# Optimization experiments

Hardware: AMD Instinct MI355X
Metric: run time of the kernel (lower is better)

Reference implementation:

```python
import jax, jax.numpy as jnp
import numpy as np

B, S, I, H = 64, 512, 1024, 1024

def setup_inputs() -> dict:
    key = jax.random.key(0)
    k1, k2, k3 = jax.random.split(key, 3)
    scale = 1.0 / np.sqrt(I + H)
    x = jax.random.normal(k1, (B, S, I), dtype=jnp.float32)
    # Stacked gate weights, order: [cell_candidate, forget, update, output]
    W = jax.random.normal(k2, (4 * H, I + H), dtype=jnp.float32) * scale
    b = jax.random.normal(k3, (4 * H,), dtype=jnp.float32) * scale
    return {"x": x, "W": W, "b": b}

def _lstm(x, W, b):
    Wx = W[:, :I]   # (4H, I)
    Wh = W[:, I:]   # (4H, H)
    # Precompute input contribution for all timesteps in one big GEMM
    xW = jnp.einsum('bsi,gi->bsg', x, Wx) + b  # (B, S, 4H)
    xW_t = jnp.transpose(xW, (1, 0, 2))        # (S, B, 4H)

    def step(carry, xw):
        h, c = carry
        pre = xw + h @ Wh.T                    # (B, 4H)
        cand, f, u, o = jnp.split(pre, 4, axis=-1)
        cand = jnp.tanh(cand)
        f = jax.nn.sigmoid(f)
        u = jax.nn.sigmoid(u)
        o = jax.nn.sigmoid(o)
        c = u * cand + f * c
        h = o * jnp.tanh(c)
        return (h, c), h

    h0 = jnp.zeros((x.shape[0], H), dtype=x.dtype)
    c0 = jnp.zeros((x.shape[0], H), dtype=x.dtype)
    (h_n, c_n), outs = jax.lax.scan(step, (h0, c0), xW_t)
    output_seq = jnp.transpose(outs, (1, 0, 2))  # (B, S, H)
    return output_seq, h_n[None], c_n[None]

def reference(x, W, b):
    return _lstm(x, W, b)
```

## Files before the change

kernel.cpp:

```cpp
#include <hip/hip_runtime.h>
#include <math.h>

typedef unsigned short ushort_t;
typedef unsigned long long u64;
typedef __attribute__((ext_vector_type(4))) float f32x4;
typedef __attribute__((ext_vector_type(8))) short s16x8;

#define XW_OFF   0UL
#define XB_OFF   268435456UL
#define WXP_OFF  335544320UL
#define WHP_OFF  343932928UL
#define BP_OFF   352321536UL
#define HBUF_OFF 352337920UL
#define CNT_OFF  352600064UL

__device__ __forceinline__ ushort_t f2bf(float f) {
  unsigned u = __builtin_bit_cast(unsigned, f);
  unsigned r = u + 0x7FFFu + ((u >> 16) & 1u);
  return (ushort_t)(r >> 16);
}
__device__ __forceinline__ float bf2f(ushort_t h) {
  unsigned u = ((unsigned)h) << 16;
  return __builtin_bit_cast(float, u);
}
__device__ __forceinline__ float sigm(float x) { return 1.f / (1.f + __expf(-x)); }
__device__ __forceinline__ float tanh_f(float x) {
  float t = __expf(-2.f * fabsf(x));
  float r = (1.f - t) / (1.f + t);
  return x >= 0.f ? r : -r;
}
__device__ __forceinline__ void gload_lds16(const void* g, void* l) {
  __builtin_amdgcn_global_load_lds(
      (const __attribute__((address_space(1))) unsigned int*)g,
      (__attribute__((address_space(3))) unsigned int*)l, 16, 0, 0);
}

__global__ __launch_bounds__(256) void convert_x(const float* __restrict__ x,
                                                 ushort_t* __restrict__ xb) {
  long gid = (long)blockIdx.x * 256 + threadIdx.x;
  const float4* x4 = (const float4*)x;
  float4 f0 = x4[gid * 2];
  float4 f1 = x4[gid * 2 + 1];
  s16x8 o;
  o[0] = (short)f2bf(f0.x); o[1] = (short)f2bf(f0.y);
  o[2] = (short)f2bf(f0.z); o[3] = (short)f2bf(f0.w);
  o[4] = (short)f2bf(f1.x); o[5] = (short)f2bf(f1.y);
  o[6] = (short)f2bf(f1.z); o[7] = (short)f2bf(f1.w);
  ((s16x8*)xb)[gid] = o;
}

__global__ __launch_bounds__(256) void prep_pack(const float* __restrict__ W,
                                                 const float* __restrict__ bias,
                                                 ushort_t* __restrict__ wxp,
                                                 ushort_t* __restrict__ whp,
                                                 float* __restrict__ bp,
                                                 ushort_t* __restrict__ hbuf,
                                                 int* __restrict__ cnt) {
  long gid = (long)blockIdx.x * 256 + threadIdx.x;
  if (gid < 524288) {
    int l = gid & 63, kc = (int)((gid >> 6) & 31), w = (int)((gid >> 11) & 3);
    int kb = (int)(gid >> 13);
    int li = l & 15, quad = l >> 4;
    int colb = w * 16 + li;
    int G = (colb & 3) * 1024 + kb * 16 + (colb >> 2);
    int kk = kc * 32 + quad * 8;
    const float* src = W + (long)G * 2048 + 1024 + kk;
    ushort_t* dst = whp + gid * 8;
#pragma unroll
    for (int j = 0; j < 8; ++j) dst[j] = f2bf(src[j]);
  } else if (gid < 1048576) {
    long id = gid - 524288;
    int k8 = (int)(id & 127);
    int R = (int)(id >> 7);
    int c = R & 63, kb = R >> 6;
    int G = (c & 3) * 1024 + kb * 16 + (c >> 2);
    const float* src = W + (long)G * 2048 + k8 * 8;
    ushort_t* dst = wxp + (long)R * 1024 + k8 * 8;
#pragma unroll
    for (int j = 0; j < 8; ++j) dst[j] = f2bf(src[j]);
  } else if (gid < 1048576 + 4096) {
    int R = (int)(gid - 1048576);
    int c = R & 63, kb = R >> 6;
    int G = (c & 3) * 1024 + kb * 16 + (c >> 2);
    bp[R] = bias[G];
  } else if (gid < 1048576 + 4096 + 8192) {
    long id = gid - 1048576 - 4096;
    s16x8 z = {0, 0, 0, 0, 0, 0, 0, 0};
    ((s16x8*)hbuf)[id] = z;
  } else if (gid < 1048576 + 4096 + 8192 + 2048) {
    cnt[gid - 1048576 - 4096 - 8192] = 0;
  }
}

__global__ __launch_bounds__(256) void lstm_phase1(const ushort_t* __restrict__ xb,
                                                   const ushort_t* __restrict__ wxp,
                                                   const float* __restrict__ bp,
                                                   ushort_t* __restrict__ xw) {
  __shared__ ushort_t As[16 * 512];
  __shared__ ushort_t Bs[16 * 512];
  int bid = blockIdx.x;
  int nt = bid & 31, mtb = bid >> 5;
  int n0 = nt * 128;
  int t0 = mtb * 2;
  int tid = threadIdx.x, w = tid >> 6, l = tid & 63;
  int quad = l >> 4, li = l & 15;
  int mh = w & 1, nh = w >> 1;
  f32x4 acc[4][4] = {};

  for (int k0 = 0; k0 < 1024; k0 += 64) {
    __syncthreads();
#pragma unroll
    for (int i = 0; i < 4; ++i) {
      int c = w * 4 + i;
      int mt = c >> 1, kcl = c & 1;
      int r = mt * 16 + li;
      int tt = t0 + (r >> 6), bb = r & 63;
      gload_lds16(xb + (long)(bb * 512 + tt) * 1024 + k0 + kcl * 32 + quad * 8,
                  &As[c * 512]);
      int rn = n0 + mt * 16 + li;
      gload_lds16(wxp + (long)rn * 1024 + k0 + kcl * 32 + quad * 8, &Bs[c * 512]);
    }
    __syncthreads();
#pragma unroll
    for (int kcl = 0; kcl < 2; ++kcl) {
      s16x8 av[4], bv[4];
#pragma unroll
      for (int i = 0; i < 4; ++i)
        av[i] = *(const s16x8*)&As[((mh * 4 + i) * 2 + kcl) * 512 + l * 8];
#pragma unroll
      for (int j = 0; j < 4; ++j)
        bv[j] = *(const s16x8*)&Bs[((nh * 4 + j) * 2 + kcl) * 512 + l * 8];
#pragma unroll
      for (int i = 0; i < 4; ++i)
#pragma unroll
        for (int j = 0; j < 4; ++j)
          acc[i][j] =
              __builtin_amdgcn_mfma_f32_16x16x32_bf16(av[i], bv[j], acc[i][j], 0, 0, 0);
    }
  }
#pragma unroll
  for (int j = 0; j < 4; ++j) {
    float bj = bp[n0 + nh * 64 + j * 16 + li];
#pragma unroll
    for (int i = 0; i < 4; ++i) {
#pragma unroll
      for (int r = 0; r < 4; ++r) {
        int lr = mh * 64 + i * 16 + quad * 4 + r;
        long off = ((long)mtb * 128 + lr) * 4096 + (n0 + nh * 64 + j * 16 + li);
        xw[off] = f2bf(acc[i][j][r] + bj);
      }
    }
  }
}

__global__ __launch_bounds__(256) void lstm_phase2(const ushort_t* __restrict__ xw,
                                                   const ushort_t* __restrict__ whp,
                                                   ushort_t* __restrict__ hbuf,
                                                   float* __restrict__ out,
                                                   int* __restrict__ counters) {
  __shared__ ushort_t Aimg[32 * 512];
  int bid = blockIdx.x;
  int gr = bid >> 6, kb = bid & 63;
  int tid = threadIdx.x, w = tid >> 6, l = tid & 63;
  int quad = l >> 4, li = l & 15;
  int colb = w * 16 + li;
  int gg = colb & 3;
  int jj = colb >> 2;
  int colh = kb * 16 + jj;

  int* flags = counters + gr * 64;

  s16x8 bfr[32];
  const ushort_t* wp = whp + (long)(kb * 4 + w) * 32 * 512 + l * 8;
#pragma unroll
  for (int kc = 0; kc < 32; ++kc) bfr[kc] = *(const s16x8*)(wp + kc * 512);

  float cst[4] = {0.f, 0.f, 0.f, 0.f};
  ushort_t pf[4];
#pragma unroll
  for (int r = 0; r < 4; ++r)
    pf[r] = xw[(long)(gr * 16 + quad * 4 + r) * 4096 + kb * 64 + colb];

  int base = l & ~3;

  for (int t = 0; t < 512; ++t) {
    int p = t & 1;
    if (t > 0) {
      int g = 0;
      for (;;) {
        int f = __hip_atomic_load(flags + l, __ATOMIC_RELAXED, __HIP_MEMORY_SCOPE_AGENT);
        if (__all(f >= t)) break;
        if (++g > 1024) break;
      }
    }
    const u64* hsrc64 = (const u64*)(hbuf + p * 65536 + gr * 16 * 1024);
    u64 hv[16];
#pragma unroll
    for (int ci = 0; ci < 8; ++ci) {
      int kc = w * 8 + ci;
      const u64* s = hsrc64 + li * 256 + kc * 8 + quad * 2;
      hv[2 * ci] = __hip_atomic_load(s, __ATOMIC_RELAXED, __HIP_MEMORY_SCOPE_AGENT);
      hv[2 * ci + 1] =
          __hip_atomic_load(s + 1, __ATOMIC_RELAXED, __HIP_MEMORY_SCOPE_AGENT);
    }
    f32x4 a0, a1, a2, a3;
#pragma unroll
    for (int r = 0; r < 4; ++r) a0[r] = bf2f(pf[r]);
    a1 = (f32x4)0.f; a2 = (f32x4)0.f; a3 = (f32x4)0.f;
    if (t < 511) {
#pragma unroll
      for (int r = 0; r < 4; ++r)
        pf[r] = xw[(long)((t + 1) * 64 + gr * 16 + quad * 4 + r) * 4096 + kb * 64 + colb];
    }
#pragma unroll
    for (int ci = 0; ci < 8; ++ci) {
      int kc = w * 8 + ci;
      u64* d = (u64*)&Aimg[kc * 512 + l * 8];
      d[0] = hv[2 * ci];
      d[1] = hv[2 * ci + 1];
    }
    __syncthreads();
#pragma unroll
    for (int kc = 0; kc < 32; ++kc) {
      s16x8 a = *(const s16x8*)&Aimg[kc * 512 + l * 8];
      switch (kc & 3) {
        case 0: a0 = __builtin_amdgcn_mfma_f32_16x16x32_bf16(a, bfr[kc], a0, 0, 0, 0); break;
        case 1: a1 = __builtin_amdgcn_mfma_f32_16x16x32_bf16(a, bfr[kc], a1, 0, 0, 0); break;
        case 2: a2 = __builtin_amdgcn_mfma_f32_16x16x32_bf16(a, bfr[kc], a2, 0, 0, 0); break;
        default: a3 = __builtin_amdgcn_mfma_f32_16x16x32_bf16(a, bfr[kc], a3, 0, 0, 0); break;
      }
    }
    f32x4 pre4 = (a0 + a1) + (a2 + a3);

    float hn[4], cn[4];
#pragma unroll
    for (int r = 0; r < 4; ++r) {
      float pre = pre4[r];
      float candp = __shfl(pre, base + 0, 64);
      float fp_ = __shfl(pre, base + 1, 64);
      float up = __shfl(pre, base + 2, 64);
      float op = __shfl(pre, base + 3, 64);
      float c_ = sigm(up) * tanh_f(candp) + sigm(fp_) * cst[r];
      cst[r] = c_;
      cn[r] = c_;
      hn[r] = sigm(op) * tanh_f(c_);
    }
    ushort_t* hdst = hbuf + (p ^ 1) * 65536;
    if (gg == 0) {
#pragma unroll
      for (int r = 0; r < 4; ++r) {
        int b = gr * 16 + quad * 4 + r;
        unsigned hb = (unsigned)f2bf(hn[r]);
        unsigned ob = __shfl_xor(hb, 4, 64);
        if ((li & 7) == 0) {
          unsigned packed = hb | (ob << 16);
          __hip_atomic_store((unsigned*)&hdst[b * 1024 + colh], packed,
                             __ATOMIC_RELAXED, __HIP_MEMORY_SCOPE_AGENT);
        }
      }
    }
    asm volatile("s_waitcnt vmcnt(0)" ::: "memory");
    __syncthreads();
    if (tid == 0)
      __hip_atomic_store(flags + kb, t + 1, __ATOMIC_RELAXED, __HIP_MEMORY_SCOPE_AGENT);
    if (gg == 0) {
#pragma unroll
      for (int r = 0; r < 4; ++r) {
        int b = gr * 16 + quad * 4 + r;
        out[((long)b * 512 + t) * 1024 + colh] = hn[r];
        if (t == 511) {
          out[33554432 + b * 1024 + colh] = hn[r];
          out[33619968 + b * 1024 + colh] = cn[r];
        }
      }
    }
  }
}

extern "C" void kernel_launch(void* const* d_in, const int* in_sizes, int n_in,
                              void* d_out, int out_size, void* d_ws, size_t ws_size,
                              hipStream_t stream) {
  const float* x = (const float*)d_in[0];
  const float* W = (const float*)d_in[1];
  const float* b = (const float*)d_in[2];
  float* out = (float*)d_out;
  char* ws = (char*)d_ws;
  ushort_t* xw = (ushort_t*)(ws + XW_OFF);
  ushort_t* xb = (ushort_t*)(ws + XB_OFF);
  ushort_t* wxp = (ushort_t*)(ws + WXP_OFF);
  ushort_t* whp = (ushort_t*)(ws + WHP_OFF);
  float* bp = (float*)(ws + BP_OFF);
  ushort_t* hbuf = (ushort_t*)(ws + HBUF_OFF);
  int* cnt = (int*)(ws + CNT_OFF);

  convert_x<<<16384, 256, 0, stream>>>(x, xb);
  prep_pack<<<4152, 256, 0, stream>>>(W, b, wxp, whp, bp, hbuf, cnt);
  lstm_phase1<<<8192, 256, 0, stream>>>(xb, wxp, bp, xw);
  lstm_phase2<<<256, 256, 0, stream>>>(xw, whp, hbuf, out, cnt);
}
```

Measured before the change: 4.920 ms.

## Use per-wave completion flags and vectorized cache-coherent loads in LSTM recurrence

Each wave now publishes its own step-completion flag, so the block-wide barrier before signalling is gone. Consumers poll four flags per lane with one dwordx4 load using the sc1 cache policy. Hidden-state reads become 16-byte loads with sc1 instead of paired 64-bit atomics, and each wave writes its four h values as a single 64-bit store. This cuts synchronization latency and memory-instruction count on the serial time-step path, at the cost of four times as many flags to poll and reliance on inline-asm coherence semantics.

```diff
diff --git a/kernel.cpp b/kernel.cpp
--- a/kernel.cpp
+++ b/kernel.cpp
@@ -5,6 +5,7 @@
 typedef unsigned long long u64;
 typedef __attribute__((ext_vector_type(4))) float f32x4;
 typedef __attribute__((ext_vector_type(8))) short s16x8;
+typedef __attribute__((ext_vector_type(4))) int s32x4;
 
 #define XW_OFF   0UL
 #define XB_OFF   268435456UL
@@ -33,6 +34,10 @@
   __builtin_amdgcn_global_load_lds(
       (const __attribute__((address_space(1))) unsigned int*)g,
       (__attribute__((address_space(3))) unsigned int*)l, 16, 0, 0);
+}
+__device__ __forceinline__ void gload16_cc(const void* p, s32x4& v) {
+  asm volatile("global_load_dwordx4 %0, %1, off sc1"
+               : "=v"(v) : "v"(p) : "memory");
 }
 
 __global__ __launch_bounds__(256) void convert_x(const float* __restrict__ x,
@@ -168,7 +173,7 @@
   int jj = colb >> 2;
   int colh = kb * 16 + jj;
 
-  int* flags = counters + gr * 64;
+  int* flags = counters + gr * 256;
 
   s16x8 bfr[32];
   const ushort_t* wp = whp + (long)(kb * 4 + w) * 32 * 512 + l * 8;
@@ -186,22 +191,22 @@
   for (int t = 0; t < 512; ++t) {
     int p = t & 1;
     if (t > 0) {
+      const void* fl4 = (const void*)(flags + l * 4);
       int g = 0;
       for (;;) {
-        int f = __hip_atomic_load(flags + l, __ATOMIC_RELAXED, __HIP_MEMORY_SCOPE_AGENT);
-        if (__all(f >= t)) break;
+        s32x4 f;
+        asm volatile("global_load_dwordx4 %0, %1, off sc1\n\ts_waitcnt vmcnt(0)"
+                     : "=v"(f) : "v"(fl4) : "memory");
+        if (__all(f[0] >= t && f[1] >= t && f[2] >= t && f[3] >= t)) break;
         if (++g > 1024) break;
       }
     }
-    const u64* hsrc64 = (const u64*)(hbuf + p * 65536 + gr * 16 * 1024);
-    u64 hv[16];
+    const char* hsrc = (const char*)hbuf + (long)p * 131072 + (long)gr * 32768;
+    s32x4 hv[8];
 #pragma unroll
     for (int ci = 0; ci < 8; ++ci) {
       int kc = w * 8 + ci;
-      const u64* s = hsrc64 + li * 256 + kc * 8 + quad * 2;
-      hv[2 * ci] = __hip_atomic_load(s, __ATOMIC_RELAXED, __HIP_MEMORY_SCOPE_AGENT);
-      hv[2 * ci + 1] =
-          __hip_atomic_load(s + 1, __ATOMIC_RELAXED, __HIP_MEMORY_SCOPE_AGENT);
+      gload16_cc(hsrc + li * 2048 + kc * 64 + quad * 16, hv[ci]);
     }
     f32x4 a0, a1, a2, a3;
 #pragma unroll
@@ -212,12 +217,12 @@
       for (int r = 0; r < 4; ++r)
         pf[r] = xw[(long)((t + 1) * 64 + gr * 16 + quad * 4 + r) * 4096 + kb * 64 + colb];
     }
+    asm volatile("s_waitcnt vmcnt(0)" ::: "memory");
+    __builtin_amdgcn_sched_barrier(0);
 #pragma unroll
     for (int ci = 0; ci < 8; ++ci) {
       int kc = w * 8 + ci;
-      u64* d = (u64*)&Aimg[kc * 512 + l * 8];
-      d[0] = hv[2 * ci];
-      d[1] = hv[2 * ci + 1];
+      *(s32x4*)&Aimg[kc * 512 + l * 8] = hv[ci];
     }
     __syncthreads();
 #pragma unroll
@@ -246,23 +251,25 @@
       hn[r] = sigm(op) * tanh_f(c_);
     }
     ushort_t* hdst = hbuf + (p ^ 1) * 65536;
-    if (gg == 0) {
-#pragma unroll
-      for (int r = 0; r < 4; ++r) {
+#pragma unroll
+    for (int r = 0; r < 4; ++r) {
+      unsigned hb = (unsigned)f2bf(hn[r]);
+      unsigned c0 = __shfl(hb, base - (l & 3) - (li & 12) + 0, 64);
+      unsigned c1 = __shfl(hb, (quad << 4) + 4, 64);
+      unsigned c2 = __shfl(hb, (quad << 4) + 8, 64);
+      unsigned c3 = __shfl(hb, (quad << 4) + 12, 64);
+      c0 = __shfl(hb, (quad << 4) + 0, 64);
+      if (li == 0) {
         int b = gr * 16 + quad * 4 + r;
-        unsigned hb = (unsigned)f2bf(hn[r]);
-        unsigned ob = __shfl_xor(hb, 4, 64);
-        if ((li & 7) == 0) {
-          unsigned packed = hb | (ob << 16);
-          __hip_atomic_store((unsigned*)&hdst[b * 1024 + colh], packed,
-                             __ATOMIC_RELAXED, __HIP_MEMORY_SCOPE_AGENT);
-        }
+        u64 packed = (u64)c0 | ((u64)c1 << 16) | ((u64)c2 << 32) | ((u64)c3 << 48);
+        __hip_atomic_store((u64*)&hdst[b * 1024 + kb * 16 + w * 4], packed,
+                           __ATOMIC_RELAXED, __HIP_MEMORY_SCOPE_AGENT);
       }
     }
     asm volatile("s_waitcnt vmcnt(0)" ::: "memory");
-    __syncthreads();
-    if (tid == 0)
-      __hip_atomic_store(flags + kb, t + 1, __ATOMIC_RELAXED, __HIP_MEMORY_SCOPE_AGENT);
+    if (l == 0)
+      __hip_atomic_store(flags + kb * 4 + w, t + 1, __ATOMIC_RELAXED,
+                         __HIP_MEMORY_SCOPE_AGENT);
     if (gg == 0) {
 #pragma unroll
       for (int r = 0; r < 4; ++r) {
```

Measured after the change: 4.566 ms. 7.2% less time.
